# Kernel tuning notes

Hardware: AMD Instinct MI355X
Metric: run time of the kernel (lower is better)

## Reference

```python
import jax, jax.numpy as jnp
import numpy as np
from jax import lax

STRIDE = (1, 1)
PADDING = ((1, 1), (1, 1))
DILATION = (1, 1)
GROUPS = 1


def setup_inputs() -> dict:
    key = jax.random.key(0)
    k1, k2, k3, k4, k5 = jax.random.split(key, 5)
    # quantized int8-ish activations/weights stored as float (as in the torch module)
    x = jax.random.randint(k1, (32, 128, 56, 56), -128, 128).astype(jnp.float32)
    weight_int = jax.random.randint(k2, (256, 128, 3, 3), -128, 128).astype(jnp.float32)
    bias_int = jax.random.randint(k3, (256,), -1024, 1024).astype(jnp.float32)
    A = jax.random.randint(k4, (256,), 1, 32768)  # per-channel requant multiplier
    N = jax.random.randint(k5, (256,), 16, 25)    # per-channel shift
    return {
        "x": x,
        "weight_int": weight_int,
        "bias_int": bias_int,
        "A": A,
        "N": N,
        "out_min": 0,
        "out_max": 255,
    }


def reference(x, weight_int, bias_int, A, N, out_min, out_max):
    # emulate torch's x.int().float() truncation casts
    xq = jnp.trunc(x)
    wq = jnp.trunc(weight_int)
    bq = jnp.trunc(bias_int)
    out = lax.conv_general_dilated(
        xq, wq,
        window_strides=STRIDE,
        padding=PADDING,
        rhs_dilation=DILATION,
        feature_group_count=GROUPS,
        dimension_numbers=("NCHW", "OIHW", "NCHW"),
    )
    out = jnp.round(out + bq[None, :, None, None])
    # out *= A ; out >>= N  (torch float rshift == divide by 2**N)
    Af = A.astype(jnp.float32)[None, :, None, None]
    Nf = N.astype(jnp.float32)[None, :, None, None]
    out = out * Af / jnp.exp2(Nf)
    if out_min >= 0:
        out = jnp.clip(jnp.round(out), float(out_min), float(out_max))
    return out
```

## Files before the change

kernel.cpp:

```cpp
#include <hip/hip_runtime.h>
#include <stdint.h>

typedef int v4i __attribute__((ext_vector_type(4)));

#define XT_H_STRIDE (66*128)
#define XT_N_STRIDE (58*66*128)
#define XT_BYTES    (32*58*66*128)
#define WQ_BYTES    (256*1152)

__device__ __forceinline__ void gload16(const void* g, void* l) {
  __builtin_amdgcn_global_load_lds(
      (const __attribute__((address_space(1))) void*)g,
      (__attribute__((address_space(3))) void*)l, 16, 0, 0);
}

__global__ __launch_bounds__(256) void xform_x(const float* __restrict__ x,
                                               char* __restrict__ xt) {
  int bid = blockIdx.x;
  int n  = bid / 58;
  int hp = bid - n * 58;
  int t = threadIdx.x;
  int srch = hp - 1;
  bool rowok = (srch >= 0) && (srch < 56);
  int srchc = rowok ? srch : 0;
  char* dstrow = xt + (size_t)n * XT_N_STRIDE + (size_t)hp * XT_H_STRIDE;
  const float* srcbase = x + (size_t)n * 128 * 3136 + (size_t)srchc * 56;
  for (int c = t; c < 528; c += 256) {
    int wp  = c >> 3;
    int cio = c & 7;
    int srw = wp - 1;
    bool ok = rowok && (srw >= 0) && (srw < 56);
    int srwc = ok ? srw : 0;
    union { signed char b[16]; v4i v; } u;
#pragma unroll
    for (int j = 0; j < 16; ++j) {
      int ci = cio * 16 + j;
      float f = ok ? srcbase[(size_t)ci * 3136 + srwc] : 0.0f;
      u.b[j] = (signed char)(int)f;
    }
    *(v4i*)(dstrow + c * 16) = u.v;
  }
}

__global__ __launch_bounds__(256) void xform_w(const float* __restrict__ wsrc,
                                               const int* __restrict__ Aq,
                                               const int* __restrict__ Nq,
                                               char* __restrict__ wq,
                                               float* __restrict__ scale) {
  int idx = blockIdx.x * 256 + threadIdx.x;
  int co = idx / 1152;
  int r  = idx - co * 1152;
  int g  = r >> 7;
  int ci = r & 127;
  int kh = g / 3;
  int kw = g - 3 * kh;
  float f = wsrc[(size_t)(co * 128 + ci) * 9 + kh * 3 + kw];
  wq[idx] = (signed char)(int)f;
  if (idx < 256) {
    scale[idx] = (float)Aq[idx] * exp2f(-(float)Nq[idx]);
  }
}

__global__ __launch_bounds__(256) void qconv_gemm(
    const char* __restrict__ xt, const char* __restrict__ wq,
    const float* __restrict__ bias, const float* __restrict__ scale,
    const int* __restrict__ pmin, const int* __restrict__ pmax,
    float* __restrict__ out) {
  __shared__ __align__(16) char As[8192];
  __shared__ __align__(16) char Bs[8192];

  int bid = blockIdx.x;
  int mt = bid & 1;
  int nt = bid >> 1;
  int n  = nt / 28;
  int ht = nt - n * 28;
  int h0 = ht * 2;
  int m0 = mt * 128;

  int t  = threadIdx.x;
  int wv = t >> 6;
  int ln = t & 63;
  int quad = ln >> 4;
  int l16  = ln & 15;
  int wm = wv & 1, wn = wv >> 1;

  const char* wbase = wq + (size_t)m0 * 1152;
  const char* xbase = xt + (size_t)n * XT_N_STRIDE + (size_t)h0 * XT_H_STRIDE;

  int a_m1 = t >> 2;
  int a_p  = (((t & 3) ^ ((t >> 3) & 3)) * 16);
  int b_w1 = t >> 2;
  char* asd1 = As + wv * 1024;
  char* asd2 = As + 4096 + wv * 1024;
  char* bsd1 = Bs + wv * 1024;
  char* bsd2 = Bs + 4096 + wv * 1024;

  v4i acc[4][4];
#pragma unroll
  for (int i = 0; i < 4; ++i)
#pragma unroll
    for (int j = 0; j < 4; ++j) {
      v4i z = {0, 0, 0, 0};
      acc[i][j] = z;
    }

  int sw = (l16 >> 1) & 3;
  int ca = (quad ^ sw) * 16;

  for (int kt = 0; kt < 18; ++kt) {
    int g  = kt >> 1;
    int c0 = (kt & 1) << 6;
    int kh = g / 3;
    int kw = g - 3 * kh;
    int k0 = kt << 6;

    if (kt) __syncthreads();

    gload16(wbase + (size_t)a_m1 * 1152 + k0 + a_p, asd1);
    gload16(wbase + (size_t)(a_m1 + 64) * 1152 + k0 + a_p, asd2);
    {
      const char* rowb = xbase + (size_t)kh * XT_H_STRIDE + (size_t)kw * 128 + c0;
      gload16(rowb + (size_t)b_w1 * 128 + a_p, bsd1);
      gload16(rowb + XT_H_STRIDE + (size_t)b_w1 * 128 + a_p, bsd2);
    }
    __syncthreads();

    v4i a[4], b[4];
#pragma unroll
    for (int i = 0; i < 4; ++i)
      a[i] = *(const v4i*)(As + (wm * 64 + i * 16 + l16) * 64 + ca);
#pragma unroll
    for (int j = 0; j < 4; ++j)
      b[j] = *(const v4i*)(Bs + (wn * 64 + j * 16 + l16) * 64 + ca);
#pragma unroll
    for (int i = 0; i < 4; ++i)
#pragma unroll
      for (int j = 0; j < 4; ++j)
        acc[i][j] = __builtin_amdgcn_mfma_i32_16x16x64_i8(a[i], b[j], acc[i][j], 0, 0, 0);
  }

  float mn = (float)pmin[0];
  float mx = (float)pmax[0];
#pragma unroll
  for (int i = 0; i < 4; ++i) {
    int co_b = m0 + wm * 64 + i * 16 + quad * 4;
#pragma unroll
    for (int r = 0; r < 4; ++r) {
      int co = co_b + r;
      float bs = bias[co];
      float sc = scale[co];
#pragma unroll
      for (int j = 0; j < 4; ++j) {
        int sl = wn * 64 + j * 16 + l16;
        int w  = sl & 63;
        int dh = sl >> 6;
        if (w < 56) {
          float f = (float)acc[i][j][r] + bs;
          f = rintf(f * sc);
          f = fminf(fmaxf(f, mn), mx);
          out[(((size_t)n * 256 + co) * 56 + (h0 + dh)) * 56 + w] = f;
        }
      }
    }
  }
}

extern "C" void kernel_launch(void* const* d_in, const int* in_sizes, int n_in,
                              void* d_out, int out_size, void* d_ws, size_t ws_size,
                              hipStream_t stream) {
  const float* x  = (const float*)d_in[0];
  const float* w  = (const float*)d_in[1];
  const float* b  = (const float*)d_in[2];
  const int*   Aq = (const int*)d_in[3];
  const int*   Nq = (const int*)d_in[4];
  const int*   mn = (const int*)d_in[5];
  const int*   mx = (const int*)d_in[6];
  float* out = (float*)d_out;

  char*  xt    = (char*)d_ws;
  char*  wq    = xt + XT_BYTES;
  float* scale = (float*)(wq + WQ_BYTES);

  hipLaunchKernelGGL(xform_x, dim3(32 * 58), dim3(256), 0, stream, x, xt);
  hipLaunchKernelGGL(xform_w, dim3(1152), dim3(256), 0, stream, w, Aq, Nq, wq, scale);
  hipLaunchKernelGGL(qconv_gemm, dim3(1792), dim3(256), 0, stream,
                     xt, wq, b, scale, mn, mx, out);
}
```

Before: 206.4 us.

## Double-buffer GEMM LDS tiles, remap blocks per XCD, coalesce input transform

The int8 conv GEMM now double-buffers its A/B LDS tiles. The next k-tile's global-to-LDS loads are issued before computing the current one, with explicit s_waitcnt vmcnt and s_barrier, so load latency overlaps with the MFMAs. Blocks are remapped so each XCD handles a contiguous range of spatial tiles, which improves L2 locality. The x transform now reads float4 vectors, packs int8 values into a padded LDS transpose buffer and writes coalesced rows, and padding rows are handled as a pure zero fill. Hand-written waitcnt and barriers risk ordering mistakes, and LDS use doubles to 32 KB per block.

Result: faster. 195.6 us (-5.2%).

```diff
diff --git a/kernel.cpp b/kernel.cpp
--- a/kernel.cpp
+++ b/kernel.cpp
@@ -1,7 +1,8 @@
 #include <hip/hip_runtime.h>
 #include <stdint.h>
 
-typedef int v4i __attribute__((ext_vector_type(4)));
+typedef int   v4i __attribute__((ext_vector_type(4)));
+typedef float v4f __attribute__((ext_vector_type(4)));
 
 #define XT_H_STRIDE (66*128)
 #define XT_N_STRIDE (58*66*128)
@@ -16,29 +17,52 @@
 
 __global__ __launch_bounds__(256) void xform_x(const float* __restrict__ x,
                                                char* __restrict__ xt) {
+  __shared__ int LB[56 * 33];
   int bid = blockIdx.x;
   int n  = bid / 58;
   int hp = bid - n * 58;
-  int t = threadIdx.x;
+  int t  = threadIdx.x;
   int srch = hp - 1;
   bool rowok = (srch >= 0) && (srch < 56);
-  int srchc = rowok ? srch : 0;
   char* dstrow = xt + (size_t)n * XT_N_STRIDE + (size_t)hp * XT_H_STRIDE;
-  const float* srcbase = x + (size_t)n * 128 * 3136 + (size_t)srchc * 56;
-  for (int c = t; c < 528; c += 256) {
-    int wp  = c >> 3;
-    int cio = c & 7;
-    int srw = wp - 1;
-    bool ok = rowok && (srw >= 0) && (srw < 56);
-    int srwc = ok ? srw : 0;
-    union { signed char b[16]; v4i v; } u;
-#pragma unroll
-    for (int j = 0; j < 16; ++j) {
-      int ci = cio * 16 + j;
-      float f = ok ? srcbase[(size_t)ci * 3136 + srwc] : 0.0f;
-      u.b[j] = (signed char)(int)f;
-    }
-    *(v4i*)(dstrow + c * 16) = u.v;
+
+  if (rowok) {
+    const float* rb = x + ((size_t)(n * 128) * 56 + srch) * 56;
+#pragma unroll
+    for (int u0 = 0; u0 < 2; ++u0) {
+      int u  = t + u0 * 256;
+      int wb = u & 15;
+      int cb = u >> 4;
+      int w0 = wb * 4, ci0 = cb * 4;
+      if (w0 < 56) {
+        int dw[4] = {0, 0, 0, 0};
+#pragma unroll
+        for (int i = 0; i < 4; ++i) {
+          v4f f = *(const v4f*)(rb + (size_t)(ci0 + i) * 3136 + w0);
+#pragma unroll
+          for (int j = 0; j < 4; ++j)
+            dw[j] |= (((int)f[j]) & 255) << (8 * i);
+        }
+#pragma unroll
+        for (int j = 0; j < 4; ++j)
+          LB[(w0 + j) * 33 + cb] = dw[j];
+      }
+    }
+    __syncthreads();
+    for (int c = t; c < 528; c += 256) {
+      int wp  = c >> 3;
+      int cio = c & 7;
+      int srw = wp - 1;
+      v4i v = {0, 0, 0, 0};
+      if (srw >= 0 && srw < 56) {
+#pragma unroll
+        for (int k = 0; k < 4; ++k) v[k] = LB[srw * 33 + cio * 4 + k];
+      }
+      *(v4i*)(dstrow + c * 16) = v;
+    }
+  } else {
+    v4i z = {0, 0, 0, 0};
+    for (int c = t; c < 528; c += 256) *(v4i*)(dstrow + c * 16) = z;
   }
 }
 
@@ -66,16 +90,18 @@
     const float* __restrict__ bias, const float* __restrict__ scale,
     const int* __restrict__ pmin, const int* __restrict__ pmax,
     float* __restrict__ out) {
-  __shared__ __align__(16) char As[8192];
-  __shared__ __align__(16) char Bs[8192];
+  __shared__ __align__(16) char As[2][8192];
+  __shared__ __align__(16) char Bs[2][8192];
 
   int bid = blockIdx.x;
-  int mt = bid & 1;
-  int nt = bid >> 1;
-  int n  = nt / 28;
-  int ht = nt - n * 28;
-  int h0 = ht * 2;
-  int m0 = mt * 128;
+  int xcd = bid & 7;
+  int q   = bid >> 3;
+  int mt  = q & 1;
+  int nt  = xcd * 112 + (q >> 1);
+  int n   = nt / 28;
+  int ht  = nt - n * 28;
+  int h0  = ht * 2;
+  int m0  = mt * 128;
 
   int t  = threadIdx.x;
   int wv = t >> 6;
@@ -90,10 +116,7 @@
   int a_m1 = t >> 2;
   int a_p  = (((t & 3) ^ ((t >> 3) & 3)) * 16);
   int b_w1 = t >> 2;
-  char* asd1 = As + wv * 1024;
-  char* asd2 = As + 4096 + wv * 1024;
-  char* bsd1 = Bs + wv * 1024;
-  char* bsd2 = Bs + 4096 + wv * 1024;
+  int ldsoff = wv * 1024;
 
   v4i acc[4][4];
 #pragma unroll
@@ -107,31 +130,38 @@
   int sw = (l16 >> 1) & 3;
   int ca = (quad ^ sw) * 16;
 
-  for (int kt = 0; kt < 18; ++kt) {
+  auto stage = [&](int kt, int p) {
     int g  = kt >> 1;
     int c0 = (kt & 1) << 6;
     int kh = g / 3;
     int kw = g - 3 * kh;
     int k0 = kt << 6;
-
-    if (kt) __syncthreads();
-
-    gload16(wbase + (size_t)a_m1 * 1152 + k0 + a_p, asd1);
-    gload16(wbase + (size_t)(a_m1 + 64) * 1152 + k0 + a_p, asd2);
-    {
-      const char* rowb = xbase + (size_t)kh * XT_H_STRIDE + (size_t)kw * 128 + c0;
-      gload16(rowb + (size_t)b_w1 * 128 + a_p, bsd1);
-      gload16(rowb + XT_H_STRIDE + (size_t)b_w1 * 128 + a_p, bsd2);
-    }
-    __syncthreads();
+    gload16(wbase + (size_t)a_m1 * 1152 + k0 + a_p, &As[p][ldsoff]);
+    gload16(wbase + (size_t)(a_m1 + 64) * 1152 + k0 + a_p, &As[p][4096 + ldsoff]);
+    const char* rowb = xbase + (size_t)kh * XT_H_STRIDE + (size_t)kw * 128 + c0;
+    gload16(rowb + (size_t)b_w1 * 128 + a_p, &Bs[p][ldsoff]);
+    gload16(rowb + XT_H_STRIDE + (size_t)b_w1 * 128 + a_p, &Bs[p][4096 + ldsoff]);
+  };
+
+  stage(0, 0);
+  for (int kt = 0; kt < 18; ++kt) {
+    int p = kt & 1;
+    asm volatile("s_barrier" ::: "memory");
+    if (kt < 17) {
+      stage(kt + 1, 1 - p);
+      asm volatile("s_waitcnt vmcnt(4)" ::: "memory");
+    } else {
+      asm volatile("s_waitcnt vmcnt(0)" ::: "memory");
+    }
+    asm volatile("s_barrier" ::: "memory");
 
     v4i a[4], b[4];
 #pragma unroll
     for (int i = 0; i < 4; ++i)
-      a[i] = *(const v4i*)(As + (wm * 64 + i * 16 + l16) * 64 + ca);
+      a[i] = *(const v4i*)(&As[p][(wm * 64 + i * 16 + l16) * 64 + ca]);
 #pragma unroll
     for (int j = 0; j < 4; ++j)
-      b[j] = *(const v4i*)(Bs + (wn * 64 + j * 16 + l16) * 64 + ca);
+      b[j] = *(const v4i*)(&Bs[p][(wn * 64 + j * 16 + l16) * 64 + ca]);
 #pragma unroll
     for (int i = 0; i < 4; ++i)
 #pragma unroll
```
